# Optimization experiments

Measured on AMD Instinct MI355X. Metric: run time of the kernel, lower is better.

Reference implementation:

```python
import jax, jax.numpy as jnp
import numpy as np
from functools import partial

# Static problem sizes (equal-sized, sorted batch assumed; batch = repeat(arange(B), NPTS))
B, NPTS, C_IN = 8, 4096, 64
M = 1024      # centroids per cloud = ratio(0.25) * NPTS
K = 64        # max_num_neighbors in radius()
R = 0.2       # ball-query radius
EPS = 1e-5    # BatchNorm eps


def fps_single(pos, m):
    """Farthest point sampling on one cloud. pos: [n,3]. Deterministic start at index 0."""
    n = pos.shape[0]
    def step(carry, _):
        dists, last = carry
        d = jnp.sum(jnp.square(pos - pos[last]), axis=-1)
        dists = jnp.minimum(dists, d)
        nxt = jnp.argmax(dists)
        return (dists, nxt), nxt
    init = (jnp.full((n,), 1e10, pos.dtype), jnp.int32(0))
    _, rest = jax.lax.scan(step, init, None, length=m - 1)
    return jnp.concatenate([jnp.zeros((1,), rest.dtype), rest])  # [m]


def bn_relu(h, W, g, b, mask):
    """Linear(no bias) + BatchNorm1d (training-mode batch stats over valid edges) + ReLU.
    h: [B,M,K,Cin], mask: [B,M,K] (1 = real neighbor edge)."""
    h = h @ W
    mk = mask[..., None]
    cnt = jnp.maximum(jnp.sum(mask), 1.0)
    mu = jnp.sum(h * mk, axis=(0, 1, 2)) / cnt
    var = jnp.sum(jnp.square(h - mu) * mk, axis=(0, 1, 2)) / cnt
    return jax.nn.relu((h - mu) * jax.lax.rsqrt(var + EPS) * g + b)


def forward(x, pos, batch, W1, g1, b1, W2, g2, b2, W3, g3, b3):
    posb = pos.reshape(B, NPTS, 3)
    xb = x.reshape(B, NPTS, C_IN)
    # --- FPS (indices are non-differentiable constants) ---
    idx = jax.lax.stop_gradient(jax.vmap(partial(fps_single, m=M))(posb))   # [B,M]
    cent = jnp.take_along_axis(posb, idx[..., None], axis=1)                # [B,M,3]
    # --- radius ball query, capped at K nearest within R (deterministic) ---
    d2 = jnp.sum(jnp.square(jax.lax.stop_gradient(cent)[:, :, None]
                            - jax.lax.stop_gradient(posb)[:, None]), axis=-1)  # [B,M,n]
    vals, nbr = jax.lax.top_k(jnp.where(d2 <= R * R, -d2, -jnp.inf), K)        # [B,M,K]
    mask = (vals > -jnp.inf).astype(pos.dtype)   # centroid itself (d2=0) always valid
    # --- gather neighbors, local MLP on [x_j, pos_j - pos_i], max-aggregate ---
    gather = jax.vmap(lambda a, i: a[i])
    pj = gather(posb, nbr)                                     # [B,M,K,3]
    xj = gather(xb, nbr)                                       # [B,M,K,C]
    h = jnp.concatenate([xj, pj - cent[:, :, None]], axis=-1)  # [B,M,K,C+3]
    h = bn_relu(h, W1, g1, b1, mask)
    h = bn_relu(h, W2, g2, b2, mask)
    h = bn_relu(h, W3, g3, b3, mask)
    x_out = jnp.max(jnp.where(mask[..., None] > 0, h, -jnp.inf), axis=2)  # [B,M,128]
    bsel = jnp.repeat(jnp.arange(B, dtype=batch.dtype), M)
    return x_out.reshape(B * M, -1), cent.reshape(B * M, 3), bsel


def setup_inputs():
    key = jax.random.key(0)
    ks = jax.random.split(key, 11)
    N = B * NPTS
    x = jax.random.normal(ks[0], (N, C_IN), jnp.float32)
    pos = jax.random.uniform(ks[1], (N, 3), jnp.float32)   # unit cube point clouds
    batch = jnp.repeat(jnp.arange(B, dtype=jnp.int32), NPTS)
    ch = [C_IN + 3, 64, 64, 128]
    def lin(k, i, o):
        return jax.random.normal(k, (i, o), jnp.float32) * (1.0 / np.sqrt(i))
    W1, W2, W3 = lin(ks[2], ch[0], ch[1]), lin(ks[3], ch[1], ch[2]), lin(ks[4], ch[2], ch[3])
    g1 = 1.0 + 0.1 * jax.random.normal(ks[5], (ch[1],), jnp.float32)
    g2 = 1.0 + 0.1 * jax.random.normal(ks[6], (ch[2],), jnp.float32)
    g3 = 1.0 + 0.1 * jax.random.normal(ks[7], (ch[3],), jnp.float32)
    b1 = 0.05 * jax.random.normal(ks[8], (ch[1],), jnp.float32)
    b2 = 0.05 * jax.random.normal(ks[9], (ch[2],), jnp.float32)
    b3 = 0.05 * jax.random.normal(ks[10], (ch[3],), jnp.float32)
    return {"x": x, "pos": pos, "batch": batch,
            "W1": W1, "g1": g1, "b1": b1,
            "W2": W2, "g2": g2, "b2": b2,
            "W3": W3, "g3": g3, "b3": b3}


def reference(x, pos, batch, W1, g1, b1, W2, g2, b2, W3, g3, b3):
    return forward(x, pos, batch, W1, g1, b1, W2, g2, b2, W3, g3, b3)
```

## Files before the change

### kernel.cpp

```cpp
#include <hip/hip_runtime.h>
#include <stdint.h>

#define NB   8
#define NPTS 4096
#define CINV 64
#define MC   1024
#define KNB  64
#define NE   (NB*MC*KNB)
#define K1   67
#define CH1  64
#define CH2  64
#define CH3  128
#define NSLOT 64
#define CAP  2048
#define NTASK (NB*MC)
#define NBLK 256

typedef unsigned short u16;
typedef unsigned int   u32;
typedef unsigned long long u64;

using f32x4  = __attribute__((ext_vector_type(4))) float;
using bf16x8 = __attribute__((ext_vector_type(8))) short;

static __device__ __forceinline__ float bf2f(u16 b){ return __uint_as_float(((u32)b)<<16); }
static __device__ __forceinline__ u16  f2bf(float f){
  u32 u = __float_as_uint(f);
  return (u16)((u + 0x7fffu + ((u>>16)&1u)) >> 16);
}
static __device__ __forceinline__ float d2ref(float ax,float ay,float az,
                                              float bx,float by,float bz){
  float dx = ax-bx, dy = ay-by, dz = az-bz;
  return __fadd_rn(__fadd_rn(__fmul_rn(dx,dx), __fmul_rn(dy,dy)), __fmul_rn(dz,dz));
}
template<int CTRL, int RMASK>
static __device__ __forceinline__ float dppaddstep(float v){
  int t = __builtin_amdgcn_update_dpp(0, __float_as_int(v), CTRL, RMASK, 0xF, false);
  return v + __int_as_float(t);
}
static __device__ __forceinline__ float dppsum16(float v){
  v = dppaddstep<0xB1,0xF>(v); v = dppaddstep<0x4E,0xF>(v);
  v = dppaddstep<0x141,0xF>(v); v = dppaddstep<0x140,0xF>(v);
  return v;
}
static __device__ __forceinline__ double kpack(float d, int ni){
  return __hiloint2double(__float_as_int(d), ni);
}
template<int CTRL, int RMASK>
static __device__ __forceinline__ double dppk64(double k){
  int hi = __double2hiint(k), lo = __double2loint(k);
  int thi = __builtin_amdgcn_update_dpp(hi, hi, CTRL, RMASK, 0xF, false);
  int tlo = __builtin_amdgcn_update_dpp(lo, lo, CTRL, RMASK, 0xF, false);
  return fmax(k, __hiloint2double(thi, tlo));
}

struct FpsL {
  float px[NPTS], py[NPTS], pz[NPTS];
  int   sIdx[MC];
  double candD[8];
  float4 cbuf[16];
};
struct WkL {
  u64   keys[CAP];
  float Hs[64*69];
  int   nbrS[64];
  float red[8][16][4];
  float cxyz[3];
  int   scnt;
  int   task;
};
union FrontL { FpsL f; WkL w; };

__global__ __launch_bounds__(512) void k_front(const float* __restrict__ x,
                                               const float* __restrict__ pos,
                                               float* __restrict__ centf,
                                               float* __restrict__ out_cent,
                                               float* __restrict__ out_bsel,
                                               const float* __restrict__ W1,
                                               float* __restrict__ Spart,
                                               u16* __restrict__ y1g,
                                               int* __restrict__ cntpc,
                                               int* __restrict__ cnt_total,
                                               int* __restrict__ progress,
                                               int* __restrict__ taskctr) {
  __shared__ FrontL L;
  const int tid = threadIdx.x;

  if (blockIdx.x < NB) {
    const int b = blockIdx.x;
    for (int i = tid; i < NPTS; i += 512) {
      size_t o = ((size_t)b*NPTS + i)*3;
      L.f.px[i] = pos[o]; L.f.py[i] = pos[o+1]; L.f.pz[i] = pos[o+2];
    }
    __syncthreads();
    if (tid >= 256) return;

    float cxr[16], cyr[16], czr[16], dist[16];
    int nio[16];
    #pragma unroll
    for (int j = 0; j < 16; ++j) {
      int p = tid*16 + j;
      cxr[j] = L.f.px[p]; cyr[j] = L.f.py[p]; czr[j] = L.f.pz[p];
      dist[j] = 1e10f;
      nio[j] = ~p;
    }
    const int lane = tid & 63, w = tid >> 6;
    float qx = L.f.px[0], qy = L.f.py[0], qz = L.f.pz[0];
    if (tid == 0) {
      L.f.sIdx[0] = 0;
      L.f.cbuf[0] = make_float4(qx, qy, qz, 0.f);
    }

    for (int it = 1; it < MC; ++it) {
      #pragma unroll
      for (int j = 0; j < 16; ++j) {
        float d = d2ref(cxr[j], cyr[j], czr[j], qx, qy, qz);
        dist[j] = fminf(dist[j], d);
      }
      double t0 = fmax(kpack(dist[0],  nio[0]),  kpack(dist[1],  nio[1]));
      double t1 = fmax(kpack(dist[2],  nio[2]),  kpack(dist[3],  nio[3]));
      double t2 = fmax(kpack(dist[4],  nio[4]),  kpack(dist[5],  nio[5]));
      double t3 = fmax(kpack(dist[6],  nio[6]),  kpack(dist[7],  nio[7]));
      double t4 = fmax(kpack(dist[8],  nio[8]),  kpack(dist[9],  nio[9]));
      double t5 = fmax(kpack(dist[10], nio[10]), kpack(dist[11], nio[11]));
      double t6 = fmax(kpack(dist[12], nio[12]), kpack(dist[13], nio[13]));
      double t7 = fmax(kpack(dist[14], nio[14]), kpack(dist[15], nio[15]));
      double u0 = fmax(t0, t1), u1 = fmax(t2, t3), u2 = fmax(t4, t5), u3 = fmax(t6, t7);
      double bk = fmax(fmax(u0, u1), fmax(u2, u3));
      bk = dppk64<0xB1,0xF>(bk);
      bk = dppk64<0x4E,0xF>(bk);
      bk = dppk64<0x141,0xF>(bk);
      bk = dppk64<0x140,0xF>(bk);
      bk = dppk64<0x142,0xA>(bk);
      bk = dppk64<0x143,0xC>(bk);
      if (lane == 63) L.f.candD[(it & 1)*4 + w] = bk;
      __syncthreads();
      double ck = L.f.candD[(it & 1)*4 + (lane & 3)];
      ck = dppk64<0xB1,0xF>(ck);
      ck = dppk64<0x4E,0xF>(ck);
      int wi = (int)(~(u32)__double2loint(ck));
      qx = L.f.px[wi]; qy = L.f.py[wi]; qz = L.f.pz[wi];
      if ((it & 15) == 0 && tid < 16) {
        int mrow = it - 16 + tid;
        float4 cc = L.f.cbuf[tid];
        int r = b*MC + mrow;
        centf[r*3+0] = cc.x; centf[r*3+1] = cc.y; centf[r*3+2] = cc.z;
        if (tid == 0)
          __hip_atomic_store(progress + b, it, __ATOMIC_RELEASE, __HIP_MEMORY_SCOPE_AGENT);
      }
      if (tid == 0) {
        L.f.sIdx[it] = wi;
        L.f.cbuf[it & 15] = make_float4(qx, qy, qz, 0.f);
      }
    }
    __syncthreads();
    if (tid < 16) {
      int mrow = MC - 16 + tid;
      float4 cc = L.f.cbuf[tid];
      int r = b*MC + mrow;
      centf[r*3+0] = cc.x; centf[r*3+1] = cc.y; centf[r*3+2] = cc.z;
      if (tid == 0)
        __hip_atomic_store(progress + b, MC, __ATOMIC_RELEASE, __HIP_MEMORY_SCOPE_AGENT);
    }
    for (int m2_ = tid; m2_ < MC; m2_ += 256) {
      int i = L.f.sIdx[m2_];
      int r = b*MC + m2_;
      out_cent[r*3+0] = L.f.px[i]; out_cent[r*3+1] = L.f.py[i]; out_cent[r*3+2] = L.f.pz[i];
      out_bsel[r] = (float)b;
    }
    return;
  }

  for (;;) {
    if (tid == 0) {
      int t = atomicAdd(taskctr, 1);
      L.w.task = t;
      if (t < NTASK) {
        int m = t >> 3, b = t & 7;
        while (__hip_atomic_load(progress + b, __ATOMIC_ACQUIRE, __HIP_MEMORY_SCOPE_AGENT) < m + 1)
          __builtin_amdgcn_s_sleep(8);
        int bm = b*MC + m;
        L.w.cxyz[0] = __hip_atomic_load(centf + bm*3 + 0, __ATOMIC_RELAXED, __HIP_MEMORY_SCOPE_AGENT);
        L.w.cxyz[1] = __hip_atomic_load(centf + bm*3 + 1, __ATOMIC_RELAXED, __HIP_MEMORY_SCOPE_AGENT);
        L.w.cxyz[2] = __hip_atomic_load(centf + bm*3 + 2, __ATOMIC_RELAXED, __HIP_MEMORY_SCOPE_AGENT);
      }
      L.w.scnt = 0;
    }
    __syncthreads();
    const int t = L.w.task;
    if (t >= NTASK) return;
    const int m = t >> 3, b = t & 7, bm = b*MC + m;
    const float cx = L.w.cxyz[0], cy = L.w.cxyz[1], cz = L.w.cxyz[2];

    for (int i = tid; i < NPTS; i += 512) {
      size_t o = ((size_t)b*NPTS + i)*3;
      float d = d2ref(cx, cy, cz, pos[o], pos[o+1], pos[o+2]);
      if (d <= 0.04f) {
        int p = atomicAdd(&L.w.scnt, 1);
        if (p < CAP) L.w.keys[p] = ((u64)__float_as_uint(d) << 32) | (u32)i;
      }
    }
    __syncthreads();
    int n = L.w.scnt; if (n > CAP) n = CAP;
    int P = 64; while (P < n) P <<= 1;
    for (int i = n + tid; i < P; i += 512) L.w.keys[i] = ~0ull;
    __syncthreads();
    for (int ks = 2; ks <= P; ks <<= 1)
      for (int js = ks >> 1; js > 0; js >>= 1) {
        for (int i = tid; i < P; i += 512) {
          int l = i ^ js;
          if (l > i) {
            u64 a = L.w.keys[i], c = L.w.keys[l];
            bool up = ((i & ks) == 0);
            if ((a > c) == up) { L.w.keys[i] = c; L.w.keys[l] = a; }
          }
        }
        __syncthreads();
      }
    const int c = n < KNB ? n : KNB;
    if (tid < KNB) L.w.nbrS[tid] = (tid < c) ? (int)(u32)(L.w.keys[tid] & 0xffffffffu) : 0;
    if (tid == 0) { cntpc[bm] = c; atomicAdd(cnt_total, c); }
    __syncthreads();

    {
      const int ge = tid >> 3, qb = tid & 7;
      const float4* xr = (const float4*)(x + ((size_t)(b*NPTS + L.w.nbrS[ge]))*CINV);
      #pragma unroll
      for (int rep = 0; rep < 2; ++rep) {
        int q = qb + rep*8;
        float4 v = xr[q];
        float* d = L.w.Hs + ge*69 + q*4;
        d[0] = v.x; d[1] = v.y; d[2] = v.z; d[3] = v.w;
      }
    }
    if (tid < 64) {
      int row = b*NPTS + L.w.nbrS[tid];
      L.w.Hs[tid*69+64] = pos[(size_t)row*3+0] - cx;
      L.w.Hs[tid*69+65] = pos[(size_t)row*3+1] - cy;
      L.w.Hs[tid*69+66] = pos[(size_t)row*3+2] - cz;
    }
    __syncthreads();

    const int edge = tid & 63;
    const int col  = __builtin_amdgcn_readfirstlane(tid >> 6);
    float acc[8];
    #pragma unroll
    for (int j = 0; j < 8; ++j) acc[j] = 0.f;
    const float* hrow = L.w.Hs + edge*69;
    const float* wcol = W1 + col*8;
    for (int k = 0; k < K1; ++k) {
      float hk = hrow[k];
      const float4* w4 = (const float4*)(wcol + k*CH1);
      float4 a = w4[0], bq = w4[1];
      acc[0] = fmaf(hk, a.x,  acc[0]); acc[1] = fmaf(hk, a.y,  acc[1]);
      acc[2] = fmaf(hk, a.z,  acc[2]); acc[3] = fmaf(hk, a.w,  acc[3]);
      acc[4] = fmaf(hk, bq.x, acc[4]); acc[5] = fmaf(hk, bq.y, acc[5]);
      acc[6] = fmaf(hk, bq.z, acc[6]); acc[7] = fmaf(hk, bq.w, acc[7]);
    }
    const bool valid = edge < c;
    #pragma unroll
    for (int j = 0; j < 8; ++j) acc[j] = valid ? acc[j] : 0.f;
    u32* dst = (u32*)(y1g + ((size_t)bm*64 + edge)*CH1 + col*8);
    #pragma unroll
    for (int j = 0; j < 4; ++j)
      dst[j] = (u32)f2bf(acc[2*j]) | ((u32)f2bf(acc[2*j+1]) << 16);
    #pragma unroll
    for (int j = 0; j < 8; ++j) {
      float s = dppsum16(acc[j]);
      float q = dppsum16(acc[j]*acc[j]);
      if ((edge & 15) == 0) {
        L.w.red[col][j][edge>>4]   = s;
        L.w.red[col][8+j][edge>>4] = q;
      }
    }
    __syncthreads();
    const int slot = bm & (NSLOT-1);
    if (tid < 64) {
      float4 g = *(const float4*)&L.w.red[tid>>3][tid&7][0];
      atomicAdd(&Spart[slot*256 + tid], (g.x+g.y)+(g.z+g.w));
    } else if (tid < 128) {
      int cc = tid - 64;
      float4 g = *(const float4*)&L.w.red[cc>>3][8+(cc&7)][0];
      atomicAdd(&Spart[slot*256 + 128 + cc], (g.x+g.y)+(g.z+g.w));
    }
  }
}

__global__ void k_wconv(const float* __restrict__ W3, const float* __restrict__ W2,
                        u16* __restrict__ W3f, u16* __restrict__ W2f) {
  int blk = blockIdx.x;
  if (blk < 32) {
    int t = blk*256 + threadIdx.x;
    int T = t >> 9, lane = (t >> 3) & 63, j = t & 7;
    int n = (T >> 1)*16 + (lane & 15);
    int k = (T & 1)*32 + (lane >> 4)*8 + j;
    W3f[t] = f2bf(W3[k*CH3 + n]);
  } else {
    int t = (blk - 32)*256 + threadIdx.x;
    int T = t >> 9, lane = (t >> 3) & 63, j = t & 7;
    int n = (T >> 1)*16 + (lane & 15);
    int k = (T & 1)*32 + (lane >> 4)*8 + j;
    W2f[t] = f2bf(W2[k*CH2 + n]);
  }
}

__global__ __launch_bounds__(256) void k_s2(const u16* __restrict__ y1g,
                                            const float* __restrict__ SC,
                                            const u16* __restrict__ W2f,
                                            const int* __restrict__ cntpc,
                                            float* __restrict__ Spart,
                                            u16* __restrict__ y2g) {
  __shared__ u16   Hb[64*72];
  __shared__ u16   Ob[64*72];
  __shared__ float ABs[128];
  __shared__ float redS[4][16][4];
  __shared__ float redQ[4][16][4];
  __shared__ int   cntS;
  const int tid = threadIdx.x, bm = blockIdx.x;
  if (tid == 0) cntS = cntpc[bm];
  if (tid < 128) ABs[tid] = SC[tid];
  __syncthreads();
  {
    const u32* yt = (const u32*)y1g + (size_t)bm*2048;
    #pragma unroll
    for (int rep = 0; rep < 8; ++rep) {
      int g = rep*256 + tid;
      int e = g >> 5, ch = (g & 31)*2;
      u32 v = yt[g];
      float lo = fmaxf(fmaf(bf2f((u16)(v & 0xffff)), ABs[ch],   ABs[64+ch]),   0.f);
      float hi = fmaxf(fmaf(bf2f((u16)(v >> 16)),    ABs[ch+1], ABs[64+ch+1]), 0.f);
      *(u32*)&Hb[e*72 + ch] = (u32)f2bf(lo) | ((u32)f2bf(hi) << 16);
    }
  }
  __syncthreads();

  const int lane = tid & 63;
  const int wv   = __builtin_amdgcn_readfirstlane(tid >> 6);
  const int r16  = lane & 15, g4 = lane >> 4;
  const int cnt  = cntS;

  bf16x8 bfr[2];
  #pragma unroll
  for (int Kt = 0; Kt < 2; ++Kt)
    bfr[Kt] = *(const bf16x8*)&W2f[((wv*2 + Kt)*64 + lane)*8];

  f32x4 acc[4];
  #pragma unroll
  for (int Mt = 0; Mt < 4; ++Mt) acc[Mt] = (f32x4){0.f, 0.f, 0.f, 0.f};

  #pragma unroll
  for (int Kt = 0; Kt < 2; ++Kt) {
    #pragma unroll
    for (int Mt = 0; Mt < 4; ++Mt) {
      bf16x8 afr = *(const bf16x8*)&Hb[(Mt*16 + r16)*72 + Kt*32 + g4*8];
      acc[Mt] = __builtin_amdgcn_mfma_f32_16x16x32_bf16(afr, bfr[Kt], acc[Mt], 0, 0, 0);
    }
  }

  {
    const int n = wv*16 + r16;
    float s = 0.f, q = 0.f;
    #pragma unroll
    for (int Mt = 0; Mt < 4; ++Mt) {
      #pragma unroll
      for (int rr = 0; rr < 4; ++rr) {
        int row = Mt*16 + g4*4 + rr;
        bool valid = row < cnt;
        float av = valid ? acc[Mt][rr] : 0.f;
        s += av; q = fmaf(av, av, q);
        Ob[row*72 + n] = f2bf(av);
      }
    }
    redS[wv][r16][g4] = s;
    redQ[wv][r16][g4] = q;
  }
  __syncthreads();
  {
    u32* yt2 = (u32*)y2g + (size_t)bm*2048;
    #pragma unroll
    for (int rep = 0; rep < 8; ++rep) {
      int g = rep*256 + tid;
      int e = g >> 5, c2 = g & 31;
      yt2[g] = *(const u32*)&Ob[e*72 + c2*2];
    }
  }
  const int slot = bm & (NSLOT-1);
  if (tid < 64) {
    float4 g = *(const float4*)&redS[tid>>4][tid&15][0];
    atomicAdd(&Spart[slot*256 + tid], (g.x+g.y)+(g.z+g.w));
  } else if (tid < 128) {
    int c = tid - 64;
    float4 g = *(const float4*)&redQ[c>>4][c&15][0];
    atomicAdd(&Spart[slot*256 + 128 + c], (g.x+g.y)+(g.z+g.w));
  }
}

__global__ __launch_bounds__(256) void k_s3(const u16* __restrict__ y2g,
                                            const float* __restrict__ SC,
                                            const u16* __restrict__ W3f,
                                            const int* __restrict__ cntpc,
                                            float* __restrict__ Spart,
                                            float* __restrict__ mxmn) {
  __shared__ u16   Hb[64*72];
  __shared__ float ABs[128];
  __shared__ float redS[4][32][4];
  __shared__ float redQ[4][32][4];
  __shared__ float redM[4][32][4];
  __shared__ float redN[4][32][4];
  __shared__ int   cntS;
  const int tid = threadIdx.x, bm = blockIdx.x;
  if (tid == 0) cntS = cntpc[bm];
  if (tid < 128) ABs[tid] = SC[128 + tid];
  __syncthreads();
  {
    const u32* yt = (const u32*)y2g + (size_t)bm*2048;
    #pragma unroll
    for (int rep = 0; rep < 8; ++rep) {
      int g = rep*256 + tid;
      int e = g >> 5, ch = (g & 31)*2;
      u32 v = yt[g];
      float lo = fmaxf(fmaf(bf2f((u16)(v & 0xffff)), ABs[ch],   ABs[64+ch]),   0.f);
      float hi = fmaxf(fmaf(bf2f((u16)(v >> 16)),    ABs[ch+1], ABs[64+ch+1]), 0.f);
      *(u32*)&Hb[e*72 + ch] = (u32)f2bf(lo) | ((u32)f2bf(hi) << 16);
    }
  }
  __syncthreads();

  const int lane = tid & 63;
  const int wv   = __builtin_amdgcn_readfirstlane(tid >> 6);
  const int r16  = lane & 15, g4 = lane >> 4;
  const int cnt  = cntS;

  bf16x8 bfr[2][2];
  #pragma unroll
  for (int Nt = 0; Nt < 2; ++Nt)
    #pragma unroll
    for (int Kt = 0; Kt < 2; ++Kt)
      bfr[Nt][Kt] = *(const bf16x8*)&W3f[(((wv*2 + Nt)*2 + Kt)*64 + lane)*8];

  f32x4 acc[4][2];
  #pragma unroll
  for (int Mt = 0; Mt < 4; ++Mt)
    #pragma unroll
    for (int Nt = 0; Nt < 2; ++Nt)
      acc[Mt][Nt] = (f32x4){0.f, 0.f, 0.f, 0.f};

  #pragma unroll
  for (int Kt = 0; Kt < 2; ++Kt) {
    #pragma unroll
    for (int Mt = 0; Mt < 4; ++Mt) {
      bf16x8 afr = *(const bf16x8*)&Hb[(Mt*16 + r16)*72 + Kt*32 + g4*8];
      #pragma unroll
      for (int Nt = 0; Nt < 2; ++Nt)
        acc[Mt][Nt] = __builtin_amdgcn_mfma_f32_16x16x32_bf16(afr, bfr[Nt][Kt],
                                                              acc[Mt][Nt], 0, 0, 0);
    }
  }

  #pragma unroll
  for (int Nt = 0; Nt < 2; ++Nt) {
    float s = 0.f, q = 0.f, mx = -1e30f, mn = 1e30f;
    #pragma unroll
    for (int Mt = 0; Mt < 4; ++Mt) {
      #pragma unroll
      for (int rr = 0; rr < 4; ++rr) {
        int row = Mt*16 + g4*4 + rr;
        float v = acc[Mt][Nt][rr];
        bool valid = row < cnt;
        float av = valid ? v : 0.f;
        s += av; q = fmaf(av, av, q);
        mx = fmaxf(mx, valid ? v : -1e30f);
        mn = fminf(mn, valid ? v :  1e30f);
      }
    }
    redS[wv][Nt*16 + r16][g4] = s;
    redQ[wv][Nt*16 + r16][g4] = q;
    redM[wv][Nt*16 + r16][g4] = mx;
    redN[wv][Nt*16 + r16][g4] = mn;
  }
  __syncthreads();
  const int slot = bm & (NSLOT-1);
  if (tid < 128) {
    float4 g = *(const float4*)&redS[tid>>5][tid&31][0];
    atomicAdd(&Spart[slot*256 + tid], (g.x+g.y)+(g.z+g.w));
    float4 gm = *(const float4*)&redM[tid>>5][tid&31][0];
    mxmn[(size_t)bm*256 + tid] = fmaxf(fmaxf(gm.x, gm.y), fmaxf(gm.z, gm.w));
  } else {
    int c = tid - 128;
    float4 g = *(const float4*)&redQ[c>>5][c&31][0];
    atomicAdd(&Spart[slot*256 + 128 + c], (g.x+g.y)+(g.z+g.w));
    float4 gm = *(const float4*)&redN[c>>5][c&31][0];
    mxmn[(size_t)bm*256 + 128 + c] = fminf(fminf(gm.x, gm.y), fminf(gm.z, gm.w));
  }
}

__global__ __launch_bounds__(128) void k_s4(const float* __restrict__ mxmn,
                                            const float* __restrict__ SC,
                                            float* __restrict__ out0) {
  const int tid = threadIdx.x, bm = blockIdx.x;
  const float a = SC[256 + tid], b = SC[384 + tid];
  const float mx = mxmn[(size_t)bm*256 + tid];
  const float mn = mxmn[(size_t)bm*256 + 128 + tid];
  const float v = (a > 0.f) ? mx : mn;
  out0[(size_t)bm*CH3 + tid] = fmaxf(fmaf(v, a, b), 0.f);
}

__global__ void k_finalize(const float* __restrict__ Spart,
                           const float* __restrict__ g, const float* __restrict__ bb,
                           const int* __restrict__ cnt_total,
                           float* __restrict__ Aout, float* __restrict__ Bout, int C) {
  int c = threadIdx.x;
  if (c < C) {
    float s = 0.f, q = 0.f;
    for (int sl = 0; sl < NSLOT; ++sl) {
      s += Spart[sl*256 + c];
      q += Spart[sl*256 + 128 + c];
    }
    float n = (float)(*cnt_total); if (n < 1.f) n = 1.f;
    float mu  = s / n;
    float var = q / n - mu*mu; if (var < 0.f) var = 0.f;
    float inv = 1.0f / sqrtf(var + 1e-5f);
    float a = g[c] * inv;
    Aout[c] = a;
    Bout[c] = bb[c] - mu*a;
  }
}

extern "C" void kernel_launch(void* const* d_in, const int* in_sizes, int n_in,
                              void* d_out, int out_size, void* d_ws, size_t ws_size,
                              hipStream_t stream) {
  (void)in_sizes; (void)n_in; (void)out_size; (void)ws_size;
  const float* x   = (const float*)d_in[0];
  const float* pos = (const float*)d_in[1];
  const float* W1  = (const float*)d_in[3];
  const float* g1  = (const float*)d_in[4];
  const float* b1  = (const float*)d_in[5];
  const float* W2  = (const float*)d_in[6];
  const float* g2  = (const float*)d_in[7];
  const float* b2  = (const float*)d_in[8];
  const float* W3  = (const float*)d_in[9];
  const float* g3  = (const float*)d_in[10];
  const float* b3  = (const float*)d_in[11];

  float* out0     = (float*)d_out;
  float* out_cent = out0 + (size_t)NB*MC*CH3;
  float* out_bsel = out_cent + (size_t)NB*MC*3;

  char* base = (char*)d_ws;
  size_t off = 0;
  auto carve = [&](size_t bytes) -> char* {
    char* p = base + off;
    off = (off + bytes + 255) & ~(size_t)255;
    return p;
  };
  float* centf = (float*)carve(sizeof(float)*NB*MC*3);
  int*   cntpc = (int*)  carve(sizeof(int)*NB*MC);
  char*  zeroblk = carve(256 + 3*NSLOT*256*sizeof(float));
  int*   cnt_total = (int*)zeroblk;
  int*   taskctr   = cnt_total + 1;
  int*   progress  = cnt_total + 2;
  float* Sp1 = (float*)(zeroblk + 256);
  float* Sp2 = Sp1 + NSLOT*256;
  float* Sp3 = Sp2 + NSLOT*256;
  float* SC = (float*)carve(512*sizeof(float));
  u16* y1g = (u16*)carve((size_t)NE*CH1*2);
  u16* y2g = (u16*)carve((size_t)NE*CH2*2);
  float* mxmn = (float*)carve((size_t)NB*MC*256*sizeof(float));
  u16* W3f = (u16*)carve(16*64*8*sizeof(u16));
  u16* W2f = (u16*)carve(8*64*8*sizeof(u16));

  hipMemsetAsync(zeroblk, 0, 256 + 3*NSLOT*256*sizeof(float), stream);
  k_wconv<<<48, 256, 0, stream>>>(W3, W2, W3f, W2f);
  k_front<<<NBLK, 512, 0, stream>>>(x, pos, centf, out_cent, out_bsel,
                                    W1, Sp1, y1g, cntpc, cnt_total, progress, taskctr);
  k_finalize<<<1, 128, 0, stream>>>(Sp1, g1, b1, cnt_total, SC + 0,   SC + 64,  CH1);
  dim3 sg(NB*MC), sb(256);
  k_s2<<<sg, sb, 0, stream>>>(y1g, SC, W2f, cntpc, Sp2, y2g);
  k_finalize<<<1, 128, 0, stream>>>(Sp2, g2, b2, cnt_total, SC + 128, SC + 192, CH2);
  k_s3<<<sg, sb, 0, stream>>>(y2g, SC, W3f, cntpc, Sp3, mxmn);
  k_finalize<<<1, 128, 0, stream>>>(Sp3, g3, b3, cnt_total, SC + 256, SC + 384, CH3);
  k_s4<<<sg, 128, 0, stream>>>(mxmn, SC, out0);
}
```

Measured before the change: 853.0 us.

## Fold BN finalize and weight conversion into neighbouring kernels

Removes the three single-block finalize launches and the weight-conversion launch. Each consumer kernel's block 0 now computes the BatchNorm scale and shift and publishes a ready flag, and the other blocks spin on that flag. Weight conversion moves into the worker blocks of the front kernel. This saves four kernel launches and their gaps, but relies on block 0 being scheduled, since every other block waits on it, and it adds a spin-wait at the start of every block.

```diff
diff --git a/kernel.cpp b/kernel.cpp
--- a/kernel.cpp
+++ b/kernel.cpp
@@ -52,6 +52,28 @@
   int thi = __builtin_amdgcn_update_dpp(hi, hi, CTRL, RMASK, 0xF, false);
   int tlo = __builtin_amdgcn_update_dpp(lo, lo, CTRL, RMASK, 0xF, false);
   return fmax(k, __hiloint2double(thi, tlo));
+}
+static __device__ __forceinline__ void bn_finalize(const float* __restrict__ Spart,
+                                                   const float* __restrict__ g,
+                                                   const float* __restrict__ bb,
+                                                   const int* __restrict__ cnt_total,
+                                                   float* __restrict__ Aout,
+                                                   float* __restrict__ Bout,
+                                                   int C, int tid) {
+  if (tid < C) {
+    float s = 0.f, q = 0.f;
+    for (int sl = 0; sl < NSLOT; ++sl) {
+      s += Spart[sl*256 + tid];
+      q += Spart[sl*256 + 128 + tid];
+    }
+    float n = (float)(*cnt_total); if (n < 1.f) n = 1.f;
+    float mu  = s / n;
+    float var = q / n - mu*mu; if (var < 0.f) var = 0.f;
+    float inv = 1.0f / sqrtf(var + 1e-5f);
+    float a = g[tid] * inv;
+    Aout[tid] = a;
+    Bout[tid] = bb[tid] - mu*a;
+  }
 }
 
 struct FpsL {
@@ -77,6 +99,10 @@
                                                float* __restrict__ out_cent,
                                                float* __restrict__ out_bsel,
                                                const float* __restrict__ W1,
+                                               const float* __restrict__ W2,
+                                               const float* __restrict__ W3,
+                                               u16* __restrict__ W2f,
+                                               u16* __restrict__ W3f,
                                                float* __restrict__ Spart,
                                                u16* __restrict__ y1g,
                                                int* __restrict__ cntpc,
@@ -171,6 +197,24 @@
     return;
   }
 
+  {
+    int wb = (int)blockIdx.x - NB;
+    if (wb < 48 && tid < 256) {
+      if (wb < 32) {
+        int t = wb*256 + tid;
+        int T = t >> 9, lane = (t >> 3) & 63, j = t & 7;
+        int n = (T >> 1)*16 + (lane & 15);
+        int k = (T & 1)*32 + (lane >> 4)*8 + j;
+        W3f[t] = f2bf(W3[k*CH3 + n]);
+      } else {
+        int t = (wb - 32)*256 + tid;
+        int T = t >> 9, lane = (t >> 3) & 63, j = t & 7;
+        int n = (T >> 1)*16 + (lane & 15);
+        int k = (T & 1)*32 + (lane >> 4)*8 + j;
+        W2f[t] = f2bf(W2[k*CH2 + n]);
+      }
+    }
+  }
   for (;;) {
     if (tid == 0) {
       int t = atomicAdd(taskctr, 1);
@@ -286,28 +330,32 @@
   }
 }
 
-__global__ void k_wconv(const float* __restrict__ W3, const float* __restrict__ W2,
-                        u16* __restrict__ W3f, u16* __restrict__ W2f) {
-  int blk = blockIdx.x;
-  if (blk < 32) {
-    int t = blk*256 + threadIdx.x;
-    int T = t >> 9, lane = (t >> 3) & 63, j = t & 7;
-    int n = (T >> 1)*16 + (lane & 15);
-    int k = (T & 1)*32 + (lane >> 4)*8 + j;
-    W3f[t] = f2bf(W3[k*CH3 + n]);
+static __device__ __forceinline__ void fin_head(const float* Sp, const float* g,
+                                                const float* bb, const int* cnt_total,
+                                                float* A, float* B, int C,
+                                                int* rdy, int tid) {
+  if (blockIdx.x == 0) {
+    bn_finalize(Sp, g, bb, cnt_total, A, B, C, tid);
+    __syncthreads();
+    if (tid == 0)
+      __hip_atomic_store(rdy, 1, __ATOMIC_RELEASE, __HIP_MEMORY_SCOPE_AGENT);
   } else {
-    int t = (blk - 32)*256 + threadIdx.x;
-    int T = t >> 9, lane = (t >> 3) & 63, j = t & 7;
-    int n = (T >> 1)*16 + (lane & 15);
-    int k = (T & 1)*32 + (lane >> 4)*8 + j;
-    W2f[t] = f2bf(W2[k*CH2 + n]);
+    if (tid == 0)
+      while (!__hip_atomic_load(rdy, __ATOMIC_ACQUIRE, __HIP_MEMORY_SCOPE_AGENT))
+        __builtin_amdgcn_s_sleep(8);
+    __syncthreads();
   }
 }
 
 __global__ __launch_bounds__(256) void k_s2(const u16* __restrict__ y1g,
-                                            const float* __restrict__ SC,
+                                            float* __restrict__ SC,
                                             const u16* __restrict__ W2f,
                                             const int* __restrict__ cntpc,
+                                            const float* __restrict__ Sp1,
+                                            const float* __restrict__ g1,
+                                            const float* __restrict__ b1,
+                                            const int* __restrict__ cnt_total,
+                                            int* __restrict__ rdy1,
                                             float* __restrict__ Spart,
                                             u16* __restrict__ y2g) {
   __shared__ u16   Hb[64*72];
@@ -317,6 +365,7 @@
   __shared__ float redQ[4][16][4];
   __shared__ int   cntS;
   const int tid = threadIdx.x, bm = blockIdx.x;
+  fin_head(Sp1, g1, b1, cnt_total, SC + 0, SC + 64, CH1, rdy1, tid);
   if (tid == 0) cntS = cntpc[bm];
   if (tid < 128) ABs[tid] = SC[tid];
   __syncthreads();
@@ -396,9 +445,14 @@
 }
 
 __global__ __launch_bounds__(256) void k_s3(const u16* __restrict__ y2g,
-                                            const float* __restrict__ SC,
+                                            float* __restrict__ SC,
                                             const u16* __restrict__ W3f,
                                             const int* __restrict__ cntpc,
+                                            const float* __restrict__ Sp2,
+                                            const float* __restrict__ g2,
+                                            const float* __restrict__ b2,
+                                            const int* __restrict__ cnt_total,
+                                            int* __restrict__ rdy2,
                                             float* __restrict__ Spart,
                                             float* __restrict__ mxmn) {
   __shared__ u16   Hb[64*72];
@@ -409,6 +463,7 @@
   __shared__ float redN[4][32][4];
   __shared__ int   cntS;
   const int tid = threadIdx.x, bm = blockIdx.x;
+  fin_head(Sp2, g2, b2, cnt_total, SC + 128, SC + 192, CH2, rdy2, tid);
   if (tid == 0) cntS = cntpc[bm];
   if (tid < 128) ABs[tid] = SC[128 + tid];
   __syncthreads();
@@ -495,35 +550,20 @@
 }
 
 __global__ __launch_bounds__(128) void k_s4(const float* __restrict__ mxmn,
-                                            const float* __restrict__ SC,
+                                            float* __restrict__ SC,
+                                            const float* __restrict__ Sp3,
+                                            const float* __restrict__ g3,
+                                            const float* __restrict__ b3,
+                                            const int* __restrict__ cnt_total,
+                                            int* __restrict__ rdy3,
                                             float* __restrict__ out0) {
   const int tid = threadIdx.x, bm = blockIdx.x;
+  fin_head(Sp3, g3, b3, cnt_total, SC + 256, SC + 384, CH3, rdy3, tid);
   const float a = SC[256 + tid], b = SC[384 + tid];
   const float mx = mxmn[(size_t)bm*256 + tid];
   const float mn = mxmn[(size_t)bm*256 + 128 + tid];
   const float v = (a > 0.f) ? mx : mn;
   out0[(size_t)bm*CH3 + tid] = fmaxf(fmaf(v, a, b), 0.f);
-}
-
-__global__ void k_finalize(const float* __restrict__ Spart,
-                           const float* __restrict__ g, const float* __restrict__ bb,
-                           const int* __restrict__ cnt_total,
-                           float* __restrict__ Aout, float* __restrict__ Bout, int C) {
-  int c = threadIdx.x;
-  if (c < C) {
-    float s = 0.f, q = 0.f;
-    for (int sl = 0; sl < NSLOT; ++sl) {
-      s += Spart[sl*256 + c];
-      q += Spart[sl*256 + 128 + c];
-    }
-    float n = (float)(*cnt_total); if (n < 1.f) n = 1.f;
-    float mu  = s / n;
-    float var = q / n - mu*mu; if (var < 0.f) var = 0.f;
-    float inv = 1.0f / sqrtf(var + 1e-5f);
-    float a = g[c] * inv;
-    Aout[c] = a;
-    Bout[c] = bb[c] - mu*a;
-  }
 }
 
 extern "C" void kernel_launch(void* const* d_in, const int* in_sizes, int n_in,
@@ -559,6 +599,9 @@
   int*   cnt_total = (int*)zeroblk;
   int*   taskctr   = cnt_total + 1;
   int*   progress  = cnt_total + 2;
+  int*   rdy1      = cnt_total + 10;
+  int*   rdy2      = cnt_total + 11;
+  int*   rdy3      = cnt_total + 12;
   float* Sp1 = (float*)(zeroblk + 256);
   float* Sp2 = Sp1 + NSLOT*256;
   float* Sp3 = Sp2 + NSLOT*256;
@@ -570,14 +613,13 @@
   u16* W2f = (u16*)carve(8*64*8*sizeof(u16));
 
   hipMemsetAsync(zeroblk, 0, 256 + 3*NSLOT*256*sizeof(float), stream);
-  k_wconv<<<48, 256, 0, stream>>>(W3, W2, W3f, W2f);
   k_front<<<NBLK, 512, 0, stream>>>(x, pos, centf, out_cent, out_bsel,
-                                    W1, Sp1, y1g, cntpc, cnt_total, progress, taskctr);
-  k_finalize<<<1, 128, 0, stream>>>(Sp1, g1, b1, cnt_total, SC + 0,   SC + 64,  CH1);
+                                    W1, W2, W3, W2f, W3f,
+                                    Sp1, y1g, cntpc, cnt_total, progress, taskctr);
   dim3 sg(NB*MC), sb(256);
-  k_s2<<<sg, sb, 0, stream>>>(y1g, SC, W2f, cntpc, Sp2, y2g);
-  k_finalize<<<1, 128, 0, stream>>>(Sp2, g2, b2, cnt_total, SC + 128, SC + 192, CH2);
-  k_s3<<<sg, sb, 0, stream>>>(y2g, SC, W3f, cntpc, Sp3, mxmn);
-  k_finalize<<<1, 128, 0, stream>>>(Sp3, g3, b3, cnt_total, SC + 256, SC + 384, CH3);
-  k_s4<<<sg, 128, 0, stream>>>(mxmn, SC, out0);
-}
+  k_s2<<<sg, sb, 0, stream>>>(y1g, SC, W2f, cntpc,
+                              Sp1, g1, b1, cnt_total, rdy1, Sp2, y2g);
+  k_s3<<<sg, sb, 0, stream>>>(y2g, SC, W3f, cntpc,
+                              Sp2, g2, b2, cnt_total, rdy2, Sp3, mxmn);
+  k_s4<<<sg, 128, 0, stream>>>(mxmn, SC, Sp3, g3, b3, cnt_total, rdy3, out0);
+}
```

Result: slower. 1.283 ms (+50.4%).
